# Kernel tuning notes

Hardware: AMD Instinct MI355X
Metric: run time of the kernel (lower is better)

Reference implementation:

```python
import jax, jax.numpy as jnp
import numpy as np

D_MODEL = 1024
D_HEAD = 64


def setup_inputs() -> dict:
    key = jax.random.key(0)
    k_x, k_q, k_k, k_v, k_o = jax.random.split(key, 5)
    scale = 1.0 / np.sqrt(D_MODEL)
    residual_stream = jax.random.normal(k_x, (4, 2048, D_MODEL), dtype=jnp.float32)
    Q = scale * jax.random.normal(k_q, (D_MODEL, D_HEAD), dtype=jnp.float32)
    K = scale * jax.random.normal(k_k, (D_MODEL, D_HEAD), dtype=jnp.float32)
    V = scale * jax.random.normal(k_v, (D_MODEL, D_HEAD), dtype=jnp.float32)
    O = scale * jax.random.normal(k_o, (D_MODEL, D_HEAD), dtype=jnp.float32)
    return {"residual_stream": residual_stream, "Q": Q, "K": K, "V": V, "O": O}


def reference(residual_stream, Q, K, V, O) -> jnp.ndarray:
    # queries/keys: [B, S, d_head]
    queries = jnp.einsum('bsd,dh->bsh', residual_stream, Q)
    keys = jnp.einsum('bsd,dh->bsh', residual_stream, K)
    # NOTE: original module applies NO 1/sqrt(d_head) scaling.
    pre_attention = jnp.einsum('bqh,bkh->bqk', queries, keys)  # [B, S, S]
    S = pre_attention.shape[-1]
    causal = jnp.tril(jnp.ones((S, S), dtype=bool))
    pre_attention = jnp.where(causal[None], pre_attention, -jnp.inf)
    attention = jax.nn.softmax(pre_attention, axis=-1)
    # x = residual @ V @ O^T : [B, S, d_model]
    x = jnp.einsum('bsd,dh,eh->bse', residual_stream, V, O)
    return jnp.einsum('bqk,bke->bqe', attention, x)
```

## Files before the change

### kernel.cpp

```cpp
#include <hip/hip_runtime.h>
#include <hip/hip_bf16.h>
#include <math.h>

#define BATCH 4
#define SEQ   2048
#define DM    1024
#define DH    64
#define NROWS (BATCH*SEQ)

typedef __hip_bfloat16 bf16;
typedef __attribute__((ext_vector_type(8))) short short8;
typedef __attribute__((ext_vector_type(4))) float floatx4;

__device__ __forceinline__ ushort f2bf(float f) {
    union { bf16 h; ushort u; } cv;
    cv.h = __float2bfloat16(f);
    return cv.u;
}
__device__ __forceinline__ float bf2f(ushort u) {
    union { unsigned int i; float f; } v; v.i = ((unsigned int)u) << 16; return v.f;
}

__device__ __forceinline__ void load_lds16(const ushort* g, ushort* l) {
    __builtin_amdgcn_global_load_lds(
        (const __attribute__((address_space(1))) unsigned int*)g,
        (__attribute__((address_space(3))) unsigned int*)l, 16, 0, 0);
}

__global__ __launch_bounds__(256) void wprep_kernel(
    const float* __restrict__ Q, const float* __restrict__ K,
    const float* __restrict__ V, ushort* __restrict__ WhT, ushort* __restrict__ WlT)
{
    int n = blockIdx.x;
    const float* W = (n < 64) ? Q : (n < 128) ? K : V;
    int c = n & 63;
    for (int k = threadIdx.x; k < DM; k += 256) {
        float w = W[k * DH + c];
        ushort hi = f2bf(w);
        WhT[n * DM + k] = hi;
        WlT[n * DM + k] = f2bf(w - bf2f(hi));
    }
}

__global__ __launch_bounds__(256) void qkv_part_kernel(
    const float* __restrict__ x, const ushort* __restrict__ WhT,
    const ushort* __restrict__ WlT, float* __restrict__ Cpart)
{
    __shared__ __align__(16) ushort Xs[2][32][34];
    __shared__ __align__(16) ushort Ws[2][192][34];
    int s0 = blockIdx.x * 32;
    int kb = blockIdx.y * 256;
    int t = threadIdx.x;
    int wave = t >> 6, lane = t & 63, m_ = lane & 15, qd = lane >> 4;
    const floatx4 z4 = {0.f, 0.f, 0.f, 0.f};
    floatx4 accq[2] = {z4, z4}, acck[2] = {z4, z4}, accv[2] = {z4, z4};
    int xr = t >> 3, xc = (t & 7) * 4;
    for (int k0 = 0; k0 < 256; k0 += 32) {
        float4 v = *(const float4*)&x[(size_t)(s0 + xr) * DM + kb + k0 + xc];
        ushort h0 = f2bf(v.x), h1 = f2bf(v.y), h2 = f2bf(v.z), h3 = f2bf(v.w);
        *(ushort4*)&Xs[0][xr][xc] = make_ushort4(h0, h1, h2, h3);
        *(ushort4*)&Xs[1][xr][xc] = make_ushort4(
            f2bf(v.x - bf2f(h0)), f2bf(v.y - bf2f(h1)),
            f2bf(v.z - bf2f(h2)), f2bf(v.w - bf2f(h3)));
        #pragma unroll
        for (int j = 0; j < 3; ++j) {
            int idx = t + j * 256, n = idx >> 2, kc = (idx & 3) * 8;
            *(uint4*)&Ws[0][n][kc] = *(const uint4*)&WhT[n * DM + kb + k0 + kc];
            *(uint4*)&Ws[1][n][kc] = *(const uint4*)&WlT[n * DM + kb + k0 + kc];
        }
        __syncthreads();
        short8 ah[2], al[2];
        #pragma unroll
        for (int mi = 0; mi < 2; ++mi) {
            ah[mi] = *(const short8*)&Xs[0][mi * 16 + m_][qd * 8];
            al[mi] = *(const short8*)&Xs[1][mi * 16 + m_][qd * 8];
        }
        int nq = wave * 16 + m_, nk = 64 + wave * 16 + m_, nv = 128 + wave * 16 + m_;
        short8 bqh = *(const short8*)&Ws[0][nq][qd * 8];
        short8 bql = *(const short8*)&Ws[1][nq][qd * 8];
        short8 bkh = *(const short8*)&Ws[0][nk][qd * 8];
        short8 bkl = *(const short8*)&Ws[1][nk][qd * 8];
        short8 bvh = *(const short8*)&Ws[0][nv][qd * 8];
        #pragma unroll
        for (int mi = 0; mi < 2; ++mi) {
            accq[mi] = __builtin_amdgcn_mfma_f32_16x16x32_bf16(ah[mi], bqh, accq[mi], 0, 0, 0);
            accq[mi] = __builtin_amdgcn_mfma_f32_16x16x32_bf16(al[mi], bqh, accq[mi], 0, 0, 0);
            accq[mi] = __builtin_amdgcn_mfma_f32_16x16x32_bf16(ah[mi], bql, accq[mi], 0, 0, 0);
            acck[mi] = __builtin_amdgcn_mfma_f32_16x16x32_bf16(ah[mi], bkh, acck[mi], 0, 0, 0);
            acck[mi] = __builtin_amdgcn_mfma_f32_16x16x32_bf16(al[mi], bkh, acck[mi], 0, 0, 0);
            acck[mi] = __builtin_amdgcn_mfma_f32_16x16x32_bf16(ah[mi], bkl, acck[mi], 0, 0, 0);
            accv[mi] = __builtin_amdgcn_mfma_f32_16x16x32_bf16(ah[mi], bvh, accv[mi], 0, 0, 0);
        }
        __syncthreads();
    }
    float* Cp = Cpart + (size_t)blockIdx.y * (NROWS * 192);
    #pragma unroll
    for (int mi = 0; mi < 2; ++mi) {
        #pragma unroll
        for (int r = 0; r < 4; ++r) {
            int row = s0 + mi * 16 + qd * 4 + r;
            float* base = Cp + (size_t)row * 192;
            base[wave * 16 + m_]       = accq[mi][r];
            base[64 + wave * 16 + m_]  = acck[mi][r];
            base[128 + wave * 16 + m_] = accv[mi][r];
        }
    }
}

__global__ __launch_bounds__(256) void qkv_reduce_kernel(
    const float* __restrict__ Cpart,
    ushort* __restrict__ qh, ushort* __restrict__ ql,
    ushort* __restrict__ kh, ushort* __restrict__ kl, ushort* __restrict__ xvh)
{
    const size_t SL = (size_t)NROWS * 192;
    int row0 = blockIdx.x * 8;
    int t = threadIdx.x;
    #pragma unroll
    for (int i = 0; i < 6; ++i) {
        int e = i * 256 + t;
        int r = e / 192, c = e - r * 192;
        size_t row = row0 + r;
        size_t off = row * 192 + c;
        float s = Cpart[off] + Cpart[SL + off] + Cpart[2 * SL + off] + Cpart[3 * SL + off];
        ushort hi = f2bf(s);
        ushort lo = f2bf(s - bf2f(hi));
        if (c < 64) {
            qh[row * 64 + c] = hi; ql[row * 64 + c] = lo;
        } else if (c < 128) {
            kh[row * 64 + c - 64] = hi; kl[row * 64 + c - 64] = lo;
        } else {
            xvh[row * 64 + c - 128] = hi;
        }
    }
}

__global__ __launch_bounds__(256) void xvo_kernel(
    const ushort* __restrict__ xvh, const float* __restrict__ O, ushort* __restrict__ xvoT)
{
    __shared__ __align__(16) ushort As[64 * 72];
    __shared__ __align__(16) ushort Bs[64 * 72];
    int e0 = blockIdx.x << 6;
    int row0 = blockIdx.y << 6;
    int t = threadIdx.x;
    int tr = t >> 2, tc = (t & 3) << 4;
    {
        const float* s1 = O + (size_t)(e0 + tr) * DH + tc;
        #pragma unroll
        for (int j = 0; j < 4; ++j) {
            float4 v1 = *(const float4*)(s1 + j * 4);
            uint2 w1;
            w1.x = (uint)f2bf(v1.x) | ((uint)f2bf(v1.y) << 16);
            w1.y = (uint)f2bf(v1.z) | ((uint)f2bf(v1.w) << 16);
            *(uint2*)&As[tr * 72 + tc + j * 4] = w1;
        }
        *(uint4*)&Bs[tr * 72 + tc]     = *(const uint4*)&xvh[(size_t)(row0 + tr) * DH + tc];
        *(uint4*)&Bs[tr * 72 + tc + 8] = *(const uint4*)&xvh[(size_t)(row0 + tr) * DH + tc + 8];
    }
    __syncthreads();
    int wave = t >> 6, lane = t & 63, m_ = lane & 15, qd = lane >> 4;
    const floatx4 z4 = {0.f, 0.f, 0.f, 0.f};
    floatx4 acc[4] = {z4, z4, z4, z4};
    #pragma unroll
    for (int k0 = 0; k0 < 64; k0 += 32) {
        short8 a = *(const short8*)&As[(wave * 16 + m_) * 72 + k0 + qd * 8];
        #pragma unroll
        for (int ni = 0; ni < 4; ++ni) {
            short8 bfr = *(const short8*)&Bs[(ni * 16 + m_) * 72 + k0 + qd * 8];
            acc[ni] = __builtin_amdgcn_mfma_f32_16x16x32_bf16(a, bfr, acc[ni], 0, 0, 0);
        }
    }
    int b = row0 >> 11, sl = row0 & 2047;
    #pragma unroll
    for (int r = 0; r < 4; ++r) {
        int e = e0 + wave * 16 + qd * 4 + r;
        ushort* orow = xvoT + (((size_t)(b * DM + e)) << 11) + sl;
        #pragma unroll
        for (int ni = 0; ni < 4; ++ni)
            orow[ni * 16 + m_] = f2bf(acc[ni][r]);
    }
}

__global__ __launch_bounds__(512) void softmax_kernel(
    const ushort* __restrict__ qh, const ushort* __restrict__ ql,
    const ushort* __restrict__ kh, const ushort* __restrict__ kl,
    ushort* __restrict__ P, float* __restrict__ lpart)
{
    __shared__ __align__(16) ushort Qs[2][32][72];
    __shared__ float lred[8][32];
    int s0g = blockIdx.x * 32;
    int split = blockIdx.y;
    int b = s0g >> 11;
    int srow = s0g & 2047;
    int t = threadIdx.x, wave = t >> 6, lane = t & 63, m_ = lane & 15, qd = lane >> 4;
    if (t < 256) {
        int r = t >> 3, c = (t & 7) * 8;
        *(uint4*)&Qs[0][r][c] = *(const uint4*)&qh[(size_t)(s0g + r) * 64 + c];
        *(uint4*)&Qs[1][r][c] = *(const uint4*)&ql[(size_t)(s0g + r) * 64 + c];
    }
    __syncthreads();
    const ushort* khb = kh + ((size_t)b << 11) * 64;
    const ushort* klb = kl + ((size_t)b << 11) * 64;
    int ntiles = ((srow + 31) >> 6) + 1;
    const floatx4 z4 = {0.f, 0.f, 0.f, 0.f};
    float lloc[2][4] = {{0.f, 0.f, 0.f, 0.f}, {0.f, 0.f, 0.f, 0.f}};
    for (int ti = 2 * wave + split; ti < ntiles; ti += 16) {
        int k0 = ti << 6;
        floatx4 acc[2][4];
        #pragma unroll
        for (int mi = 0; mi < 2; ++mi)
            #pragma unroll
            for (int ni = 0; ni < 4; ++ni) acc[mi][ni] = z4;
        #pragma unroll
        for (int kk = 0; kk < 2; ++kk) {
            short8 ah0 = *(const short8*)&Qs[0][0 * 16 + m_][kk * 32 + qd * 8];
            short8 ah1 = *(const short8*)&Qs[0][1 * 16 + m_][kk * 32 + qd * 8];
            short8 al0 = *(const short8*)&Qs[1][0 * 16 + m_][kk * 32 + qd * 8];
            short8 al1 = *(const short8*)&Qs[1][1 * 16 + m_][kk * 32 + qd * 8];
            #pragma unroll
            for (int ni = 0; ni < 4; ++ni) {
                size_t koff = (size_t)(k0 + ni * 16 + m_) * 64 + kk * 32 + qd * 8;
                short8 bh = *(const short8*)&khb[koff];
                short8 bl = *(const short8*)&klb[koff];
                acc[0][ni] = __builtin_amdgcn_mfma_f32_16x16x32_bf16(ah0, bh, acc[0][ni], 0, 0, 0);
                acc[0][ni] = __builtin_amdgcn_mfma_f32_16x16x32_bf16(al0, bh, acc[0][ni], 0, 0, 0);
                acc[0][ni] = __builtin_amdgcn_mfma_f32_16x16x32_bf16(ah0, bl, acc[0][ni], 0, 0, 0);
                acc[1][ni] = __builtin_amdgcn_mfma_f32_16x16x32_bf16(ah1, bh, acc[1][ni], 0, 0, 0);
                acc[1][ni] = __builtin_amdgcn_mfma_f32_16x16x32_bf16(al1, bh, acc[1][ni], 0, 0, 0);
                acc[1][ni] = __builtin_amdgcn_mfma_f32_16x16x32_bf16(ah1, bl, acc[1][ni], 0, 0, 0);
            }
        }
        #pragma unroll
        for (int mi = 0; mi < 2; ++mi)
            #pragma unroll
            for (int ni = 0; ni < 4; ++ni) {
                int kc = k0 + ni * 16 + m_;
                #pragma unroll
                for (int r = 0; r < 4; ++r) {
                    int row = srow + mi * 16 + qd * 4 + r;
                    float p = (kc <= row) ? __expf(acc[mi][ni][r]) : 0.f;
                    lloc[mi][r] += p;
                    P[(size_t)(s0g + mi * 16 + qd * 4 + r) * 2048 + kc] = f2bf(p);
                }
            }
    }
    #pragma unroll
    for (int d = 1; d < 16; d <<= 1)
        #pragma unroll
        for (int mi = 0; mi < 2; ++mi)
            #pragma unroll
            for (int r = 0; r < 4; ++r)
                lloc[mi][r] += __shfl_xor(lloc[mi][r], d);
    if (m_ == 0)
        #pragma unroll
        for (int mi = 0; mi < 2; ++mi)
            #pragma unroll
            for (int r = 0; r < 4; ++r)
                lred[wave][mi * 16 + qd * 4 + r] = lloc[mi][r];
    __syncthreads();
    if (t < 32) {
        float s = 0.f;
        #pragma unroll
        for (int w = 0; w < 8; ++w) s += lred[w][t];
        lpart[split * NROWS + s0g + t] = s;
    }
}

__global__ __launch_bounds__(256) void av_kernel(
    const ushort* __restrict__ P, const ushort* __restrict__ xvoT,
    float* __restrict__ out, const float* __restrict__ lpart)
{
    __shared__ __align__(16) ushort As[2][64 * 64];
    __shared__ __align__(16) ushort Bs[2][128 * 64];
    int bid = blockIdx.x;
    int my = 31 - (bid >> 5);
    int r5 = bid & 31;
    int b = r5 & 3;
    int n0 = (r5 >> 2) << 7;
    int m0 = my << 6;
    int t = threadIdx.x, wave = t >> 6, lane = t & 63, m_ = lane & 15, qd = lane >> 4;
    const ushort* Pb = P + ((size_t)b << 22);
    const ushort* Xb = xvoT + ((size_t)(b * DM) << 11);
    const floatx4 z4 = {0.f, 0.f, 0.f, 0.f};
    floatx4 acc[2][4];
    #pragma unroll
    for (int mi = 0; mi < 2; ++mi)
        #pragma unroll
        for (int ni = 0; ni < 4; ++ni) acc[mi][ni] = z4;
    int mb = (wave >> 1) << 5;
    int nb = (wave & 1) << 6;
    int drow = lane >> 3;
    int dlc = ((lane & 7) ^ drow) << 3;
    int ntk = my + 1;
    #define AV_STAGE(ti, buf)                                                   \
        {                                                                       \
            int k0_ = (ti) << 6;                                                \
            _Pragma("unroll")                                                   \
            for (int i_ = 0; i_ < 6; ++i_) {                                    \
                int c_ = wave * 6 + i_;                                         \
                if (c_ < 8)                                                     \
                    load_lds16(Pb + (size_t)(m0 + c_ * 8 + drow) * SEQ + k0_ + dlc, \
                               &As[buf][c_ * 512]);                             \
                else                                                            \
                    load_lds16(Xb + (size_t)(n0 + (c_ - 8) * 8 + drow) * SEQ + k0_ + dlc, \
                               &Bs[buf][(c_ - 8) * 512]);                       \
            }                                                                   \
        }
    AV_STAGE(0, 0)
    for (int ti = 0; ti < ntk; ++ti) {
        __syncthreads();
        if (ti + 1 < ntk) AV_STAGE(ti + 1, (ti + 1) & 1)
        int bufi = ti & 1;
        short8 a[2][2], bb[2][4];
        #pragma unroll
        for (int kk = 0; kk < 2; ++kk) {
            #pragma unroll
            for (int mi = 0; mi < 2; ++mi) {
                int row = mb + mi * 16 + m_;
                a[kk][mi] = *(const short8*)&As[bufi][row * 64 + (((kk << 2) + qd) ^ (row & 7)) * 8];
            }
            #pragma unroll
            for (int ni = 0; ni < 4; ++ni) {
                int row = nb + ni * 16 + m_;
                bb[kk][ni] = *(const short8*)&Bs[bufi][row * 64 + (((kk << 2) + qd) ^ (row & 7)) * 8];
            }
        }
        #pragma unroll
        for (int kk = 0; kk < 2; ++kk)
            #pragma unroll
            for (int mi = 0; mi < 2; ++mi)
                #pragma unroll
                for (int ni = 0; ni < 4; ++ni)
                    acc[mi][ni] = __builtin_amdgcn_mfma_f32_16x16x32_bf16(a[kk][mi], bb[kk][ni], acc[mi][ni], 0, 0, 0);
    }
    float* ob = out + (size_t)b * SEQ * DM;
    #pragma unroll
    for (int mi = 0; mi < 2; ++mi) {
        #pragma unroll
        for (int r = 0; r < 4; ++r) {
            int row = m0 + mb + mi * 16 + qd * 4 + r;
            int rowg = (b << 11) + row;
            float scale = 1.f / (lpart[rowg] + lpart[NROWS + rowg]);
            float* orow = ob + (size_t)row * DM + n0 + nb;
            #pragma unroll
            for (int ni = 0; ni < 4; ++ni)
                orow[ni * 16 + m_] = acc[mi][ni][r] * scale;
        }
    }
}

extern "C" void kernel_launch(void* const* d_in, const int* in_sizes, int n_in,
                              void* d_out, int out_size, void* d_ws, size_t ws_size,
                              hipStream_t stream) {
    const float* x = (const float*)d_in[0];
    const float* Q = (const float*)d_in[1];
    const float* K = (const float*)d_in[2];
    const float* V = (const float*)d_in[3];
    const float* O = (const float*)d_in[4];
    float* out = (float*)d_out;

    char* ws = (char*)d_ws;
    ushort* qh   = (ushort*)(ws);
    ushort* ql   = (ushort*)(ws + (1ull  << 20));
    ushort* kh   = (ushort*)(ws + (2ull  << 20));
    ushort* kl   = (ushort*)(ws + (3ull  << 20));
    ushort* xvh  = (ushort*)(ws + (4ull  << 20));
    ushort* WhT  = (ushort*)(ws + (5ull  << 20));
    ushort* WlT  = (ushort*)(ws + (5ull  << 20) + (512ull << 10));
    float*  lpart = (float*)(ws + (6ull  << 20));
    ushort* xvoT = (ushort*)(ws + (7ull  << 20));
    ushort* Pbuf = (ushort*)(ws + (23ull << 20));
    float*  Cpart = (float*)(ws + (23ull << 20));

    wprep_kernel<<<192, 256, 0, stream>>>(Q, K, V, WhT, WlT);
    qkv_part_kernel<<<dim3(NROWS / 32, 4), 256, 0, stream>>>(x, WhT, WlT, Cpart);
    qkv_reduce_kernel<<<NROWS / 8, 256, 0, stream>>>(Cpart, qh, ql, kh, kl, xvh);
    xvo_kernel<<<dim3(DM / 64, NROWS / 64), 256, 0, stream>>>(xvh, O, xvoT);
    softmax_kernel<<<dim3(NROWS / 32, 2), 512, 0, stream>>>(qh, ql, kh, kl, Pbuf, lpart);
    av_kernel<<<32 * 8 * 4, 256, 0, stream>>>(Pbuf, xvoT, out, lpart);
}
```

Baseline: 177.3 us.

## Pair short and long causal row tiles per block in softmax and AV kernels

Both the score/exp kernel and the AV kernel now give each block two query row tiles, one near the top and one near the bottom of the causal triangle, so every block does about the same amount of work. The AV kernel shares each loaded xvo tile between both tiles' accumulators and launches half as many blocks. The softmax kernel uses 256 threads with a 4-way key split, and the AV epilogue sums four partial row sums instead of two. The cost is more registers for the second accumulator set and more LDS per block, which may lower occupancy.

```diff
diff --git a/kernel.cpp b/kernel.cpp
--- a/kernel.cpp
+++ b/kernel.cpp
@@ -180,30 +180,41 @@
     }
 }
 
-__global__ __launch_bounds__(512) void softmax_kernel(
+__global__ __launch_bounds__(256) void softmax_kernel(
     const ushort* __restrict__ qh, const ushort* __restrict__ ql,
     const ushort* __restrict__ kh, const ushort* __restrict__ kl,
     ushort* __restrict__ P, float* __restrict__ lpart)
 {
-    __shared__ __align__(16) ushort Qs[2][32][72];
-    __shared__ float lred[8][32];
-    int s0g = blockIdx.x * 32;
-    int split = blockIdx.y;
-    int b = s0g >> 11;
-    int srow = s0g & 2047;
+    __shared__ __align__(16) ushort Qs[2][2][32][72];
+    __shared__ float lred[4][2][32];
+    int pp = blockIdx.x & 31, b = blockIdx.x >> 5, s = blockIdx.y;
+    int jA = pp, jB = 63 - pp;
+    int srowA = jA << 5, srowB = jB << 5;
+    int s0gA = (b << 11) + srowA, s0gB = (b << 11) + srowB;
     int t = threadIdx.x, wave = t >> 6, lane = t & 63, m_ = lane & 15, qd = lane >> 4;
-    if (t < 256) {
-        int r = t >> 3, c = (t & 7) * 8;
-        *(uint4*)&Qs[0][r][c] = *(const uint4*)&qh[(size_t)(s0g + r) * 64 + c];
-        *(uint4*)&Qs[1][r][c] = *(const uint4*)&ql[(size_t)(s0g + r) * 64 + c];
+    #pragma unroll
+    for (int i = 0; i < 4; ++i) {
+        int idx = i * 256 + t;
+        int tile = idx >> 9, hl = (idx >> 8) & 1, r = (idx >> 3) & 31, c = (idx & 7) * 8;
+        const ushort* src = (hl ? ql : qh) + (size_t)((tile ? s0gB : s0gA) + r) * 64 + c;
+        *(uint4*)&Qs[tile][hl][r][c] = *(const uint4*)src;
     }
     __syncthreads();
     const ushort* khb = kh + ((size_t)b << 11) * 64;
     const ushort* klb = kl + ((size_t)b << 11) * 64;
-    int ntiles = ((srow + 31) >> 6) + 1;
+    int ntA = (jA >> 1) + 1, ntB = (jB >> 1) + 1;
+    int nAs = (ntA > s) ? (((ntA - 1 - s) >> 2) + 1) : 0;
+    int nBs = (ntB > s) ? (((ntB - 1 - s) >> 2) + 1) : 0;
+    int ntot = nAs + nBs;
     const floatx4 z4 = {0.f, 0.f, 0.f, 0.f};
-    float lloc[2][4] = {{0.f, 0.f, 0.f, 0.f}, {0.f, 0.f, 0.f, 0.f}};
-    for (int ti = 2 * wave + split; ti < ntiles; ti += 16) {
+    float llA[2][4] = {{0.f,0.f,0.f,0.f},{0.f,0.f,0.f,0.f}};
+    float llB[2][4] = {{0.f,0.f,0.f,0.f},{0.f,0.f,0.f,0.f}};
+    for (int it = wave; it < ntot; it += 4) {
+        int isA = (it < nAs);
+        int ti = isA ? (s + 4 * it) : (s + 4 * (it - nAs));
+        int srow = isA ? srowA : srowB;
+        int s0g = isA ? s0gA : s0gB;
+        int tidx = isA ? 0 : 1;
         int k0 = ti << 6;
         floatx4 acc[2][4];
         #pragma unroll
@@ -212,10 +223,10 @@
             for (int ni = 0; ni < 4; ++ni) acc[mi][ni] = z4;
         #pragma unroll
         for (int kk = 0; kk < 2; ++kk) {
-            short8 ah0 = *(const short8*)&Qs[0][0 * 16 + m_][kk * 32 + qd * 8];
-            short8 ah1 = *(const short8*)&Qs[0][1 * 16 + m_][kk * 32 + qd * 8];
-            short8 al0 = *(const short8*)&Qs[1][0 * 16 + m_][kk * 32 + qd * 8];
-            short8 al1 = *(const short8*)&Qs[1][1 * 16 + m_][kk * 32 + qd * 8];
+            short8 ah0 = *(const short8*)&Qs[tidx][0][0 * 16 + m_][kk * 32 + qd * 8];
+            short8 ah1 = *(const short8*)&Qs[tidx][0][1 * 16 + m_][kk * 32 + qd * 8];
+            short8 al0 = *(const short8*)&Qs[tidx][1][0 * 16 + m_][kk * 32 + qd * 8];
+            short8 al1 = *(const short8*)&Qs[tidx][1][1 * 16 + m_][kk * 32 + qd * 8];
             #pragma unroll
             for (int ni = 0; ni < 4; ++ni) {
                 size_t koff = (size_t)(k0 + ni * 16 + m_) * 64 + kk * 32 + qd * 8;
@@ -238,7 +249,7 @@
                 for (int r = 0; r < 4; ++r) {
                     int row = srow + mi * 16 + qd * 4 + r;
                     float p = (kc <= row) ? __expf(acc[mi][ni][r]) : 0.f;
-                    lloc[mi][r] += p;
+                    if (isA) llA[mi][r] += p; else llB[mi][r] += p;
                     P[(size_t)(s0g + mi * 16 + qd * 4 + r) * 2048 + kc] = f2bf(p);
                 }
             }
@@ -248,20 +259,24 @@
         #pragma unroll
         for (int mi = 0; mi < 2; ++mi)
             #pragma unroll
-            for (int r = 0; r < 4; ++r)
-                lloc[mi][r] += __shfl_xor(lloc[mi][r], d);
+            for (int r = 0; r < 4; ++r) {
+                llA[mi][r] += __shfl_xor(llA[mi][r], d);
+                llB[mi][r] += __shfl_xor(llB[mi][r], d);
+            }
     if (m_ == 0)
         #pragma unroll
         for (int mi = 0; mi < 2; ++mi)
             #pragma unroll
-            for (int r = 0; r < 4; ++r)
-                lred[wave][mi * 16 + qd * 4 + r] = lloc[mi][r];
+            for (int r = 0; r < 4; ++r) {
+                lred[wave][0][mi * 16 + qd * 4 + r] = llA[mi][r];
+                lred[wave][1][mi * 16 + qd * 4 + r] = llB[mi][r];
+            }
     __syncthreads();
-    if (t < 32) {
-        float s = 0.f;
-        #pragma unroll
-        for (int w = 0; w < 8; ++w) s += lred[w][t];
-        lpart[split * NROWS + s0g + t] = s;
+    if (t < 64) {
+        int tile = t >> 5, row = t & 31;
+        float sm = lred[0][tile][row] + lred[1][tile][row]
+                 + lred[2][tile][row] + lred[3][tile][row];
+        lpart[(size_t)s * NROWS + (tile ? s0gB : s0gA) + row] = sm;
     }
 }
 
@@ -269,81 +284,97 @@
     const ushort* __restrict__ P, const ushort* __restrict__ xvoT,
     float* __restrict__ out, const float* __restrict__ lpart)
 {
-    __shared__ __align__(16) ushort As[2][64 * 64];
+    __shared__ __align__(16) ushort AL[2][64 * 64];
+    __shared__ __align__(16) ushort AS[2][64 * 64];
     __shared__ __align__(16) ushort Bs[2][128 * 64];
     int bid = blockIdx.x;
-    int my = 31 - (bid >> 5);
+    int p = bid >> 5;
     int r5 = bid & 31;
     int b = r5 & 3;
     int n0 = (r5 >> 2) << 7;
-    int m0 = my << 6;
+    int m0L = (31 - p) << 6, m0S = p << 6;
+    int ntk = 32 - p;
+    int ntkS = p + 1;
     int t = threadIdx.x, wave = t >> 6, lane = t & 63, m_ = lane & 15, qd = lane >> 4;
     const ushort* Pb = P + ((size_t)b << 22);
     const ushort* Xb = xvoT + ((size_t)(b * DM) << 11);
     const floatx4 z4 = {0.f, 0.f, 0.f, 0.f};
-    floatx4 acc[2][4];
+    floatx4 accL[2][4], accS[2][4];
     #pragma unroll
     for (int mi = 0; mi < 2; ++mi)
         #pragma unroll
-        for (int ni = 0; ni < 4; ++ni) acc[mi][ni] = z4;
+        for (int ni = 0; ni < 4; ++ni) { accL[mi][ni] = z4; accS[mi][ni] = z4; }
     int mb = (wave >> 1) << 5;
     int nb = (wave & 1) << 6;
     int drow = lane >> 3;
     int dlc = ((lane & 7) ^ drow) << 3;
-    int ntk = my + 1;
-    #define AV_STAGE(ti, buf)                                                   \
-        {                                                                       \
-            int k0_ = (ti) << 6;                                                \
-            _Pragma("unroll")                                                   \
-            for (int i_ = 0; i_ < 6; ++i_) {                                    \
-                int c_ = wave * 6 + i_;                                         \
-                if (c_ < 8)                                                     \
-                    load_lds16(Pb + (size_t)(m0 + c_ * 8 + drow) * SEQ + k0_ + dlc, \
-                               &As[buf][c_ * 512]);                             \
-                else                                                            \
+    #define AV_STAGE(kt, buf)                                                    \
+        {                                                                        \
+            int k0_ = (kt) << 6;                                                 \
+            _Pragma("unroll")                                                    \
+            for (int i_ = 0; i_ < 8; ++i_) {                                     \
+                int c_ = wave * 8 + i_;                                          \
+                if (c_ < 8)                                                      \
+                    load_lds16(Pb + (size_t)(m0L + c_ * 8 + drow) * SEQ + k0_ + dlc, \
+                               &AL[buf][c_ * 512]);                              \
+                else if (c_ < 24)                                                \
                     load_lds16(Xb + (size_t)(n0 + (c_ - 8) * 8 + drow) * SEQ + k0_ + dlc, \
-                               &Bs[buf][(c_ - 8) * 512]);                       \
-            }                                                                   \
+                               &Bs[buf][(c_ - 8) * 512]);                        \
+                else if ((kt) < ntkS)                                            \
+                    load_lds16(Pb + (size_t)(m0S + (c_ - 24) * 8 + drow) * SEQ + k0_ + dlc, \
+                               &AS[buf][(c_ - 24) * 512]);                       \
+            }                                                                    \
         }
     AV_STAGE(0, 0)
-    for (int ti = 0; ti < ntk; ++ti) {
+    for (int kt = 0; kt < ntk; ++kt) {
         __syncthreads();
-        if (ti + 1 < ntk) AV_STAGE(ti + 1, (ti + 1) & 1)
-        int bufi = ti & 1;
-        short8 a[2][2], bb[2][4];
+        if (kt + 1 < ntk) AV_STAGE(kt + 1, (kt + 1) & 1)
+        int bufi = kt & 1;
         #pragma unroll
         for (int kk = 0; kk < 2; ++kk) {
+            short8 bb[4];
+            #pragma unroll
+            for (int ni = 0; ni < 4; ++ni) {
+                int row = nb + ni * 16 + m_;
+                bb[ni] = *(const short8*)&Bs[bufi][row * 64 + (((kk << 2) + qd) ^ (row & 7)) * 8];
+            }
             #pragma unroll
             for (int mi = 0; mi < 2; ++mi) {
                 int row = mb + mi * 16 + m_;
-                a[kk][mi] = *(const short8*)&As[bufi][row * 64 + (((kk << 2) + qd) ^ (row & 7)) * 8];
-            }
-            #pragma unroll
-            for (int ni = 0; ni < 4; ++ni) {
-                int row = nb + ni * 16 + m_;
-                bb[kk][ni] = *(const short8*)&Bs[bufi][row * 64 + (((kk << 2) + qd) ^ (row & 7)) * 8];
-            }
-        }
-        #pragma unroll
-        for (int kk = 0; kk < 2; ++kk)
-            #pragma unroll
-            for (int mi = 0; mi < 2; ++mi)
+                short8 aL = *(const short8*)&AL[bufi][row * 64 + (((kk << 2) + qd) ^ (row & 7)) * 8];
                 #pragma unroll
                 for (int ni = 0; ni < 4; ++ni)
-                    acc[mi][ni] = __builtin_amdgcn_mfma_f32_16x16x32_bf16(a[kk][mi], bb[kk][ni], acc[mi][ni], 0, 0, 0);
+                    accL[mi][ni] = __builtin_amdgcn_mfma_f32_16x16x32_bf16(aL, bb[ni], accL[mi][ni], 0, 0, 0);
+            }
+            if (kt < ntkS) {
+                #pragma unroll
+                for (int mi = 0; mi < 2; ++mi) {
+                    int row = mb + mi * 16 + m_;
+                    short8 aS = *(const short8*)&AS[bufi][row * 64 + (((kk << 2) + qd) ^ (row & 7)) * 8];
+                    #pragma unroll
+                    for (int ni = 0; ni < 4; ++ni)
+                        accS[mi][ni] = __builtin_amdgcn_mfma_f32_16x16x32_bf16(aS, bb[ni], accS[mi][ni], 0, 0, 0);
+                }
+            }
+        }
     }
     float* ob = out + (size_t)b * SEQ * DM;
     #pragma unroll
     for (int mi = 0; mi < 2; ++mi) {
         #pragma unroll
         for (int r = 0; r < 4; ++r) {
-            int row = m0 + mb + mi * 16 + qd * 4 + r;
-            int rowg = (b << 11) + row;
-            float scale = 1.f / (lpart[rowg] + lpart[NROWS + rowg]);
-            float* orow = ob + (size_t)row * DM + n0 + nb;
-            #pragma unroll
-            for (int ni = 0; ni < 4; ++ni)
-                orow[ni * 16 + m_] = acc[mi][ni][r] * scale;
+            int rowL = m0L + mb + mi * 16 + qd * 4 + r;
+            int rowS = m0S + mb + mi * 16 + qd * 4 + r;
+            int rgL = (b << 11) + rowL, rgS = (b << 11) + rowS;
+            float scL = 1.f / (lpart[rgL] + lpart[NROWS + rgL] + lpart[2*NROWS + rgL] + lpart[3*NROWS + rgL]);
+            float scS = 1.f / (lpart[rgS] + lpart[NROWS + rgS] + lpart[2*NROWS + rgS] + lpart[3*NROWS + rgS]);
+            float* orL = ob + (size_t)rowL * DM + n0 + nb;
+            float* orS = ob + (size_t)rowS * DM + n0 + nb;
+            #pragma unroll
+            for (int ni = 0; ni < 4; ++ni) {
+                orL[ni * 16 + m_] = accL[mi][ni][r] * scL;
+                orS[ni * 16 + m_] = accS[mi][ni][r] * scS;
+            }
         }
     }
 }
@@ -375,6 +406,6 @@
     qkv_part_kernel<<<dim3(NROWS / 32, 4), 256, 0, stream>>>(x, WhT, WlT, Cpart);
     qkv_reduce_kernel<<<NROWS / 8, 256, 0, stream>>>(Cpart, qh, ql, kh, kl, xvh);
     xvo_kernel<<<dim3(DM / 64, NROWS / 64), 256, 0, stream>>>(xvh, O, xvoT);
-    softmax_kernel<<<dim3(NROWS / 32, 2), 512, 0, stream>>>(qh, ql, kh, kl, Pbuf, lpart);
-    av_kernel<<<32 * 8 * 4, 256, 0, stream>>>(Pbuf, xvoT, out, lpart);
-}
+    softmax_kernel<<<dim3(32 * BATCH, 4), 256, 0, stream>>>(qh, ql, kh, kl, Pbuf, lpart);
+    av_kernel<<<16 * 8 * 4, 256, 0, stream>>>(Pbuf, xvoT, out, lpart);
+}
```

After: 175.2 us. About the same (-1.2%).
